# Optimization experiments

Measured on AMD Instinct MI355X. Metric: run time of the kernel, lower is better.

The kernel has to match this reference:

```python
import jax, jax.numpy as jnp
import numpy as np

V, D, B, L = 100000, 64, 4096, 200

def setup_inputs() -> dict:
    key = jax.random.key(0)
    ks = jax.random.split(key, 10)
    s = 0.05  # keep activations in a sane range for sigmoid
    return {
        "item_ids": jax.random.randint(ks[0], (B,), 0, V),
        "history": jax.random.randint(ks[1], (B, L), 0, V),
        "hist_len": jax.random.randint(ks[2], (B,), 1, L + 1),
        "emb_table": jax.random.normal(ks[3], (V, D), jnp.float32) * s,
        "aW1": jax.random.normal(ks[4], (3 * D, D), jnp.float32) * s,
        "ab1": jnp.zeros((D,), jnp.float32),
        "aW2": jax.random.normal(ks[5], (D, 1), jnp.float32) * s,
        "ab2": jnp.zeros((1,), jnp.float32),
        "fW1": jax.random.normal(ks[6], (3 * D, 128), jnp.float32) * s,
        "fb1": jnp.zeros((128,), jnp.float32),
        "fW2": jax.random.normal(ks[7], (128, 64), jnp.float32) * s,
        "fb2": jnp.zeros((64,), jnp.float32),
        "fW3": jax.random.normal(ks[8], (64, 1), jnp.float32) * s,
        "fb3": jnp.zeros((1,), jnp.float32),
    }

def reference(item_ids, history, hist_len, emb_table, aW1, ab1, aW2, ab2,
              fW1, fb1, fW2, fb2, fW3, fb3):
    target = emb_table[item_ids]                      # [B, D]
    hist = emb_table[history]                         # [B, L, D]
    # original pads short histories with zero rows -> zero the padded tail
    mask = (jnp.arange(hist.shape[1])[None, :] < hist_len[:, None]).astype(hist.dtype)
    hist = hist * mask[..., None]
    tgt = jnp.broadcast_to(target[:, None, :], hist.shape)     # [B, L, D]
    # attention_fc takes 3*D features: (hist, target, hist*target)
    feat = jnp.concatenate([hist, tgt, hist * tgt], axis=-1)   # [B, L, 3D]
    h = jax.nn.relu(feat @ aW1 + ab1)                 # [B, L, D]
    scores = (h @ aW2 + ab2)[..., 0]                  # [B, L]
    # faithful to original: softmax over full padded length (no length mask)
    w = jax.nn.softmax(scores, axis=1)
    pooled = jnp.einsum('bl,bld->bd', w, hist)        # [B, D]
    comb = jnp.concatenate([target, pooled, pooled - target], axis=-1)  # [B, 3D]
    z = jax.nn.relu(comb @ fW1 + fb1)
    z = jax.nn.relu(z @ fW2 + fb2)
    return jax.nn.sigmoid(z @ fW3 + fb3)              # [B, 1]
```

## Files before the change

### kernel.cpp

```cpp
#include <hip/hip_runtime.h>
#include <hip/hip_bf16.h>

#define NV 100000
#define ND 64
#define NB 4096
#define NL 200

typedef __bf16 bf16_t;
typedef __bf16 bf16x8 __attribute__((ext_vector_type(8)));
typedef float f32x4 __attribute__((ext_vector_type(4)));

#define HSTRIDE 72
#define MT 13

__global__ __launch_bounds__(256)
void din_kernel1(const int* __restrict__ item_ids,
                 const int* __restrict__ history,
                 const int* __restrict__ hist_len,
                 const float* __restrict__ emb,
                 const float* __restrict__ aW1,
                 const float* __restrict__ ab1,
                 const float* __restrict__ aW2,
                 float* __restrict__ comb_ws)
{
    __shared__ __align__(16) bf16_t histA[208 * HSTRIDE];
    __shared__ __align__(16) bf16_t wbT[64 * HSTRIDE];
    __shared__ float tgt[64];
    __shared__ float cb[64];
    __shared__ __align__(16) float scores[208];
    __shared__ float wts[208];
    __shared__ float pp[4 * 64];
    __shared__ float red[8];
    __shared__ float pooled[64];

    const int b   = blockIdx.x;
    const int tid = threadIdx.x;
    const int len = hist_len[b];

    if (tid < 64) tgt[tid] = emb[(long)item_ids[b] * ND + tid];

    {
        const int p     = tid & 3;
        const int lbase = tid >> 2;
        for (int pass = 0; pass < 4; ++pass) {
            int l = pass * 64 + lbase;
            if (l < 208) {
                bf16x8 o0 = (bf16x8)(bf16_t)0.f;
                bf16x8 o1 = (bf16x8)(bf16_t)0.f;
                if (l < NL && l < len) {
                    int idx = history[b * NL + l];
                    const float* src = emb + (long)idx * ND + p * 16;
                    f32x4 a0 = *(const f32x4*)(src);
                    f32x4 a1 = *(const f32x4*)(src + 4);
                    f32x4 a2 = *(const f32x4*)(src + 8);
                    f32x4 a3 = *(const f32x4*)(src + 12);
                    for (int i = 0; i < 4; ++i) {
                        o0[i]     = (bf16_t)a0[i];
                        o0[i + 4] = (bf16_t)a1[i];
                        o1[i]     = (bf16_t)a2[i];
                        o1[i + 4] = (bf16_t)a3[i];
                    }
                }
                bf16_t* dst = &histA[l * HSTRIDE + p * 16];
                *(bf16x8*)(dst)     = o0;
                *(bf16x8*)(dst + 8) = o1;
            }
        }
    }
    __syncthreads();

    {
        const int n  = tid & 63;
        const int kp = tid >> 6;
        float csum = 0.f;
        for (int i = 0; i < 16; ++i) {
            int k = kp * 16 + i;
            float tk = tgt[k];
            float w  = aW1[k * 64 + n] + tk * aW1[(128 + k) * 64 + n];
            wbT[n * HSTRIDE + k] = (bf16_t)w;
            csum += tk * aW1[(64 + k) * 64 + n];
        }
        pp[kp * 64 + n] = csum;
    }
    __syncthreads();
    if (tid < 64) cb[tid] = ab1[tid] + pp[tid] + pp[64 + tid] + pp[128 + tid] + pp[192 + tid];
    __syncthreads();

    {
        const int wave = tid >> 6;
        const int lane = tid & 63;
        const int col  = lane & 15;
        const int quad = lane >> 4;

        bf16x8 bfrag[4][2];
        for (int nt = 0; nt < 4; ++nt)
            for (int kb = 0; kb < 2; ++kb)
                bfrag[nt][kb] = *(const bf16x8*)&wbT[(nt * 16 + col) * HSTRIDE + kb * 32 + quad * 8];
        float cvals[4], a2vals[4];
        for (int nt = 0; nt < 4; ++nt) {
            cvals[nt]  = cb[nt * 16 + col];
            a2vals[nt] = aW2[nt * 16 + col];
        }

        for (int mt = wave; mt < MT; mt += 4) {
            const bf16_t* arow = &histA[(mt * 16 + col) * HSTRIDE + quad * 8];
            bf16x8 af0 = *(const bf16x8*)(arow);
            bf16x8 af1 = *(const bf16x8*)(arow + 32);
            float sc[4] = {0.f, 0.f, 0.f, 0.f};
            for (int nt = 0; nt < 4; ++nt) {
                f32x4 acc = {0.f, 0.f, 0.f, 0.f};
                acc = __builtin_amdgcn_mfma_f32_16x16x32_bf16(af0, bfrag[nt][0], acc, 0, 0, 0);
                acc = __builtin_amdgcn_mfma_f32_16x16x32_bf16(af1, bfrag[nt][1], acc, 0, 0, 0);
                for (int i = 0; i < 4; ++i) {
                    float h = acc[i] + cvals[nt];
                    h = h > 0.f ? h : 0.f;
                    sc[i] += h * a2vals[nt];
                }
            }
            for (int off = 1; off < 16; off <<= 1)
                for (int i = 0; i < 4; ++i)
                    sc[i] += __shfl_xor(sc[i], off, 64);
            if (col == 0) {
                f32x4 outv = {sc[0], sc[1], sc[2], sc[3]};
                *(f32x4*)&scores[mt * 16 + quad * 4] = outv;
            }
        }
    }
    __syncthreads();

    {
        float s = (tid < NL) ? scores[tid] : -1e30f;
        float m = s;
        for (int off = 32; off > 0; off >>= 1) m = fmaxf(m, __shfl_xor(m, off, 64));
        if ((tid & 63) == 0) red[tid >> 6] = m;
        __syncthreads();
        m = fmaxf(fmaxf(red[0], red[1]), fmaxf(red[2], red[3]));
        float e = (tid < NL) ? __expf(s - m) : 0.f;
        float ssum = e;
        for (int off = 32; off > 0; off >>= 1) ssum += __shfl_xor(ssum, off, 64);
        if ((tid & 63) == 0) red[4 + (tid >> 6)] = ssum;
        __syncthreads();
        float tot = red[4] + red[5] + red[6] + red[7];
        if (tid < NL) wts[tid] = e / tot;
    }
    __syncthreads();

    {
        const int wave = tid >> 6, lane = tid & 63;
        float acc = 0.f;
        for (int i = 0; i < 50; ++i) {
            int l = wave * 50 + i;
            float wl = wts[l];
            acc += wl * (float)histA[l * HSTRIDE + lane];
        }
        pp[wave * 64 + lane] = acc;
    }
    __syncthreads();
    if (tid < 64) pooled[tid] = pp[tid] + pp[64 + tid] + pp[128 + tid] + pp[192 + tid];
    __syncthreads();

    if (tid < 192) {
        float v;
        if (tid < 64)       v = tgt[tid];
        else if (tid < 128) v = pooled[tid - 64];
        else                v = pooled[tid - 128] - tgt[tid - 128];
        comb_ws[(long)b * 192 + tid] = v;
    }
}

__global__ __launch_bounds__(256)
void din_kernel2(const float* __restrict__ comb,
                 const float* __restrict__ fW1, const float* __restrict__ fb1,
                 const float* __restrict__ fW2, const float* __restrict__ fb2,
                 const float* __restrict__ fW3, const float* __restrict__ fb3,
                 float* __restrict__ out)
{
    __shared__ float z1s[16 * 130];
    __shared__ float z2s[16 * 66];
    const int tid = threadIdx.x;
    const int r   = tid >> 4;
    const int c   = tid & 15;
    const int row = blockIdx.x * 16 + r;

    float acc[8];
    for (int jj = 0; jj < 8; ++jj) acc[jj] = fb1[c * 8 + jj];
    for (int i = 0; i < 192; ++i) {
        float cm = comb[(long)row * 192 + i];
        const float* wr = fW1 + i * 128 + c * 8;
        f32x4 w0 = *(const f32x4*)(wr);
        f32x4 w1 = *(const f32x4*)(wr + 4);
        for (int jj = 0; jj < 4; ++jj) {
            acc[jj]     += cm * w0[jj];
            acc[jj + 4] += cm * w1[jj];
        }
    }
    for (int jj = 0; jj < 8; ++jj) z1s[r * 130 + c * 8 + jj] = fmaxf(acc[jj], 0.f);
    __syncthreads();

    float a2[4];
    for (int jj = 0; jj < 4; ++jj) a2[jj] = fb2[c * 4 + jj];
    for (int i = 0; i < 128; ++i) {
        float zv = z1s[r * 130 + i];
        f32x4 w = *(const f32x4*)(fW2 + i * 64 + c * 4);
        for (int jj = 0; jj < 4; ++jj) a2[jj] += zv * w[jj];
    }
    for (int jj = 0; jj < 4; ++jj) z2s[r * 66 + c * 4 + jj] = fmaxf(a2[jj], 0.f);
    __syncthreads();

    if (c == 0) {
        float s = fb3[0];
        for (int j = 0; j < 64; ++j) s += z2s[r * 66 + j] * fW3[j];
        out[row] = 1.f / (1.f + __expf(-s));
    }
}

extern "C" void kernel_launch(void* const* d_in, const int* in_sizes, int n_in,
                              void* d_out, int out_size, void* d_ws, size_t ws_size,
                              hipStream_t stream) {
    const int*   item_ids = (const int*)d_in[0];
    const int*   history  = (const int*)d_in[1];
    const int*   hist_len = (const int*)d_in[2];
    const float* emb      = (const float*)d_in[3];
    const float* aW1      = (const float*)d_in[4];
    const float* ab1      = (const float*)d_in[5];
    const float* aW2      = (const float*)d_in[6];
    const float* fW1      = (const float*)d_in[8];
    const float* fb1      = (const float*)d_in[9];
    const float* fW2      = (const float*)d_in[10];
    const float* fb2      = (const float*)d_in[11];
    const float* fW3      = (const float*)d_in[12];
    const float* fb3      = (const float*)d_in[13];

    float* comb = (float*)d_ws;

    din_kernel1<<<NB, 256, 0, stream>>>(item_ids, history, hist_len, emb,
                                        aW1, ab1, aW2, comb);
    din_kernel2<<<NB / 16, 256, 0, stream>>>(comb, fW1, fb1, fW2, fb2, fW3, fb3,
                                             (float*)d_out);
}
```

Baseline: 164.5 us.

## Stream history embeddings into MFMA registers instead of staging them in LDS

Drops the 208-row bf16 history tile from shared memory. Each wave now loads its embedding rows straight into registers in MFMA fragment layout and overlaps the first tile's gather with the weight-folding step. The pooling stage re-reads embeddings from global memory through saved indices, which adds a second gather but should cut LDS use and raise occupancy (launch bounds now ask for 5 blocks). It also vectorises the weight fold with shuffle reductions and rewrites the MLP kernel so each wave handles one row.

```diff
diff --git a/kernel.cpp b/kernel.cpp
--- a/kernel.cpp
+++ b/kernel.cpp
@@ -5,15 +5,14 @@
 #define ND 64
 #define NB 4096
 #define NL 200
+#define WST 72
 
 typedef __bf16 bf16_t;
 typedef __bf16 bf16x8 __attribute__((ext_vector_type(8)));
-typedef float f32x4 __attribute__((ext_vector_type(4)));
-
-#define HSTRIDE 72
-#define MT 13
-
-__global__ __launch_bounds__(256)
+typedef __bf16 bf16x4 __attribute__((ext_vector_type(4)));
+typedef float  f32x4  __attribute__((ext_vector_type(4)));
+
+__global__ __launch_bounds__(256, 5)
 void din_kernel1(const int* __restrict__ item_ids,
                  const int* __restrict__ history,
                  const int* __restrict__ hist_len,
@@ -23,122 +22,154 @@
                  const float* __restrict__ aW2,
                  float* __restrict__ comb_ws)
 {
-    __shared__ __align__(16) bf16_t histA[208 * HSTRIDE];
-    __shared__ __align__(16) bf16_t wbT[64 * HSTRIDE];
+    __shared__ __align__(16) bf16_t wbT[64 * WST];
+    __shared__ __align__(16) float scores[208];
+    __shared__ float wts[208];
+    __shared__ int   hidx[208];
+    __shared__ float pp[4 * 64];
     __shared__ float tgt[64];
     __shared__ float cb[64];
-    __shared__ __align__(16) float scores[208];
-    __shared__ float wts[208];
-    __shared__ float pp[4 * 64];
     __shared__ float red[8];
     __shared__ float pooled[64];
 
-    const int b   = blockIdx.x;
-    const int tid = threadIdx.x;
-    const int len = hist_len[b];
-
-    if (tid < 64) tgt[tid] = emb[(long)item_ids[b] * ND + tid];
+    const int b    = blockIdx.x;
+    const int tid  = threadIdx.x;
+    const int item = item_ids[b];
+    const int len  = hist_len[b];
+    const int wave = tid >> 6, lane = tid & 63;
+    const int col  = lane & 15, quad = lane >> 4;
+
+    if (tid < 64) tgt[tid] = emb[(long)item * ND + tid];
 
     {
-        const int p     = tid & 3;
-        const int lbase = tid >> 2;
-        for (int pass = 0; pass < 4; ++pass) {
-            int l = pass * 64 + lbase;
-            if (l < 208) {
-                bf16x8 o0 = (bf16x8)(bf16_t)0.f;
-                bf16x8 o1 = (bf16x8)(bf16_t)0.f;
-                if (l < NL && l < len) {
-                    int idx = history[b * NL + l];
-                    const float* src = emb + (long)idx * ND + p * 16;
-                    f32x4 a0 = *(const f32x4*)(src);
-                    f32x4 a1 = *(const f32x4*)(src + 4);
-                    f32x4 a2 = *(const f32x4*)(src + 8);
-                    f32x4 a3 = *(const f32x4*)(src + 12);
-                    for (int i = 0; i < 4; ++i) {
-                        o0[i]     = (bf16_t)a0[i];
-                        o0[i + 4] = (bf16_t)a1[i];
-                        o1[i]     = (bf16_t)a2[i];
-                        o1[i + 4] = (bf16_t)a3[i];
-                    }
-                }
-                bf16_t* dst = &histA[l * HSTRIDE + p * 16];
-                *(bf16x8*)(dst)     = o0;
-                *(bf16x8*)(dst + 8) = o1;
+        const int n4 = (tid & 15) * 4;
+        const int kp = tid >> 4;
+        f32x4 t4  = *(const f32x4*)(emb + (long)item * ND + kp * 4);
+        f32x4 wa0 = *(const f32x4*)(aW1 + (kp * 4 + 0) * 64 + n4);
+        f32x4 wa1 = *(const f32x4*)(aW1 + (kp * 4 + 1) * 64 + n4);
+        f32x4 wa2 = *(const f32x4*)(aW1 + (kp * 4 + 2) * 64 + n4);
+        f32x4 wa3 = *(const f32x4*)(aW1 + (kp * 4 + 3) * 64 + n4);
+        f32x4 wb0 = *(const f32x4*)(aW1 + (64 + kp * 4 + 0) * 64 + n4);
+        f32x4 wb1 = *(const f32x4*)(aW1 + (64 + kp * 4 + 1) * 64 + n4);
+        f32x4 wb2 = *(const f32x4*)(aW1 + (64 + kp * 4 + 2) * 64 + n4);
+        f32x4 wb3 = *(const f32x4*)(aW1 + (64 + kp * 4 + 3) * 64 + n4);
+        f32x4 wc0 = *(const f32x4*)(aW1 + (128 + kp * 4 + 0) * 64 + n4);
+        f32x4 wc1 = *(const f32x4*)(aW1 + (128 + kp * 4 + 1) * 64 + n4);
+        f32x4 wc2 = *(const f32x4*)(aW1 + (128 + kp * 4 + 2) * 64 + n4);
+        f32x4 wc3 = *(const f32x4*)(aW1 + (128 + kp * 4 + 3) * 64 + n4);
+
+        f32x4 c4;
+        #pragma unroll
+        for (int j = 0; j < 4; ++j) {
+            bf16x4 w;
+            w[0] = (bf16_t)(wa0[j] + t4[0] * wc0[j]);
+            w[1] = (bf16_t)(wa1[j] + t4[1] * wc1[j]);
+            w[2] = (bf16_t)(wa2[j] + t4[2] * wc2[j]);
+            w[3] = (bf16_t)(wa3[j] + t4[3] * wc3[j]);
+            *(bf16x4*)&wbT[(n4 + j) * WST + kp * 4] = w;
+            c4[j] = t4[0] * wb0[j] + t4[1] * wb1[j] + t4[2] * wb2[j] + t4[3] * wb3[j];
+        }
+        #pragma unroll
+        for (int j = 0; j < 4; ++j) {
+            c4[j] += __shfl_xor(c4[j], 16, 64);
+            c4[j] += __shfl_xor(c4[j], 32, 64);
+        }
+        if (lane < 16) *(f32x4*)&pp[wave * 64 + n4] = c4;
+    }
+
+    const int  l0   = wave * 16 + col;
+    const int  lc0  = l0 < NL ? l0 : NL - 1;
+    const int  idx0 = history[b * NL + lc0];
+    const bool v0   = l0 < len;
+    const float* s0 = emb + (long)idx0 * ND + quad * 8;
+    f32x4 pa0 = *(const f32x4*)(s0);
+    f32x4 pa1 = *(const f32x4*)(s0 + 4);
+    f32x4 pa2 = *(const f32x4*)(s0 + 32);
+    f32x4 pa3 = *(const f32x4*)(s0 + 36);
+
+    __syncthreads();
+
+    if (tid < 64) cb[tid] = ab1[tid] + pp[tid] + pp[64 + tid] + pp[128 + tid] + pp[192 + tid];
+
+    bf16x8 bfrag[4][2];
+    #pragma unroll
+    for (int nt = 0; nt < 4; ++nt)
+        #pragma unroll
+        for (int kb = 0; kb < 2; ++kb)
+            bfrag[nt][kb] = *(const bf16x8*)&wbT[(nt * 16 + col) * WST + kb * 32 + quad * 8];
+    float a2vals[4];
+    #pragma unroll
+    for (int nt = 0; nt < 4; ++nt) a2vals[nt] = aW2[nt * 16 + col];
+
+    __syncthreads();
+    float cvals[4];
+    #pragma unroll
+    for (int nt = 0; nt < 4; ++nt) cvals[nt] = cb[nt * 16 + col];
+
+    auto do_tile = [&](int mt, f32x4 a0, f32x4 a1, f32x4 a2, f32x4 a3, bool valid) {
+        bf16x8 af0, af1;
+        #pragma unroll
+        for (int i = 0; i < 4; ++i) {
+            af0[i]     = (bf16_t)a0[i];
+            af0[i + 4] = (bf16_t)a1[i];
+            af1[i]     = (bf16_t)a2[i];
+            af1[i + 4] = (bf16_t)a3[i];
+        }
+        if (!valid) { af0 = (bf16x8)(bf16_t)0.f; af1 = (bf16x8)(bf16_t)0.f; }
+        float sc[4] = {0.f, 0.f, 0.f, 0.f};
+        #pragma unroll
+        for (int nt = 0; nt < 4; ++nt) {
+            f32x4 acc = {0.f, 0.f, 0.f, 0.f};
+            acc = __builtin_amdgcn_mfma_f32_16x16x32_bf16(af0, bfrag[nt][0], acc, 0, 0, 0);
+            acc = __builtin_amdgcn_mfma_f32_16x16x32_bf16(af1, bfrag[nt][1], acc, 0, 0, 0);
+            #pragma unroll
+            for (int i = 0; i < 4; ++i) {
+                float h = acc[i] + cvals[nt];
+                h = h > 0.f ? h : 0.f;
+                sc[i] += h * a2vals[nt];
             }
         }
-    }
-    __syncthreads();
-
-    {
-        const int n  = tid & 63;
-        const int kp = tid >> 6;
-        float csum = 0.f;
-        for (int i = 0; i < 16; ++i) {
-            int k = kp * 16 + i;
-            float tk = tgt[k];
-            float w  = aW1[k * 64 + n] + tk * aW1[(128 + k) * 64 + n];
-            wbT[n * HSTRIDE + k] = (bf16_t)w;
-            csum += tk * aW1[(64 + k) * 64 + n];
-        }
-        pp[kp * 64 + n] = csum;
-    }
-    __syncthreads();
-    if (tid < 64) cb[tid] = ab1[tid] + pp[tid] + pp[64 + tid] + pp[128 + tid] + pp[192 + tid];
-    __syncthreads();
-
-    {
-        const int wave = tid >> 6;
-        const int lane = tid & 63;
-        const int col  = lane & 15;
-        const int quad = lane >> 4;
-
-        bf16x8 bfrag[4][2];
-        for (int nt = 0; nt < 4; ++nt)
-            for (int kb = 0; kb < 2; ++kb)
-                bfrag[nt][kb] = *(const bf16x8*)&wbT[(nt * 16 + col) * HSTRIDE + kb * 32 + quad * 8];
-        float cvals[4], a2vals[4];
-        for (int nt = 0; nt < 4; ++nt) {
-            cvals[nt]  = cb[nt * 16 + col];
-            a2vals[nt] = aW2[nt * 16 + col];
-        }
-
-        for (int mt = wave; mt < MT; mt += 4) {
-            const bf16_t* arow = &histA[(mt * 16 + col) * HSTRIDE + quad * 8];
-            bf16x8 af0 = *(const bf16x8*)(arow);
-            bf16x8 af1 = *(const bf16x8*)(arow + 32);
-            float sc[4] = {0.f, 0.f, 0.f, 0.f};
-            for (int nt = 0; nt < 4; ++nt) {
-                f32x4 acc = {0.f, 0.f, 0.f, 0.f};
-                acc = __builtin_amdgcn_mfma_f32_16x16x32_bf16(af0, bfrag[nt][0], acc, 0, 0, 0);
-                acc = __builtin_amdgcn_mfma_f32_16x16x32_bf16(af1, bfrag[nt][1], acc, 0, 0, 0);
-                for (int i = 0; i < 4; ++i) {
-                    float h = acc[i] + cvals[nt];
-                    h = h > 0.f ? h : 0.f;
-                    sc[i] += h * a2vals[nt];
-                }
-            }
-            for (int off = 1; off < 16; off <<= 1)
-                for (int i = 0; i < 4; ++i)
-                    sc[i] += __shfl_xor(sc[i], off, 64);
-            if (col == 0) {
-                f32x4 outv = {sc[0], sc[1], sc[2], sc[3]};
-                *(f32x4*)&scores[mt * 16 + quad * 4] = outv;
-            }
-        }
+        #pragma unroll
+        for (int off = 1; off < 16; off <<= 1)
+            #pragma unroll
+            for (int i = 0; i < 4; ++i) sc[i] += __shfl_xor(sc[i], off, 64);
+        if (col == 0) {
+            f32x4 outv = {sc[0], sc[1], sc[2], sc[3]};
+            *(f32x4*)&scores[mt * 16 + quad * 4] = outv;
+        }
+    };
+
+    if (quad == 0 && l0 < NL) hidx[l0] = idx0;
+    do_tile(wave, pa0, pa1, pa2, pa3, v0);
+
+    for (int mt = wave + 4; mt < 13; mt += 4) {
+        const int  l    = mt * 16 + col;
+        const int  lc   = l < NL ? l : NL - 1;
+        const int  idxv = history[b * NL + lc];
+        const bool vv   = l < len;
+        const float* sp = emb + (long)idxv * ND + quad * 8;
+        f32x4 a0 = *(const f32x4*)(sp);
+        f32x4 a1 = *(const f32x4*)(sp + 4);
+        f32x4 a2 = *(const f32x4*)(sp + 32);
+        f32x4 a3 = *(const f32x4*)(sp + 36);
+        if (quad == 0 && l < NL) hidx[l] = idxv;
+        do_tile(mt, a0, a1, a2, a3, vv);
     }
     __syncthreads();
 
     {
         float s = (tid < NL) ? scores[tid] : -1e30f;
         float m = s;
+        #pragma unroll
         for (int off = 32; off > 0; off >>= 1) m = fmaxf(m, __shfl_xor(m, off, 64));
-        if ((tid & 63) == 0) red[tid >> 6] = m;
+        if (lane == 0) red[wave] = m;
         __syncthreads();
         m = fmaxf(fmaxf(red[0], red[1]), fmaxf(red[2], red[3]));
         float e = (tid < NL) ? __expf(s - m) : 0.f;
         float ssum = e;
+        #pragma unroll
         for (int off = 32; off > 0; off >>= 1) ssum += __shfl_xor(ssum, off, 64);
-        if ((tid & 63) == 0) red[4 + (tid >> 6)] = ssum;
+        if (lane == 0) red[4 + wave] = ssum;
         __syncthreads();
         float tot = red[4] + red[5] + red[6] + red[7];
         if (tid < NL) wts[tid] = e / tot;
@@ -146,12 +177,10 @@
     __syncthreads();
 
     {
-        const int wave = tid >> 6, lane = tid & 63;
         float acc = 0.f;
-        for (int i = 0; i < 50; ++i) {
-            int l = wave * 50 + i;
-            float wl = wts[l];
-            acc += wl * (float)histA[l * HSTRIDE + lane];
+        for (int l = wave; l < NL; l += 4) {
+            float wl = (l < len) ? wts[l] : 0.f;
+            acc += wl * emb[(long)hidx[l] * ND + lane];
         }
         pp[wave * 64 + lane] = acc;
     }
@@ -175,43 +204,36 @@
                  const float* __restrict__ fW3, const float* __restrict__ fb3,
                  float* __restrict__ out)
 {
-    __shared__ float z1s[16 * 130];
-    __shared__ float z2s[16 * 66];
-    const int tid = threadIdx.x;
-    const int r   = tid >> 4;
-    const int c   = tid & 15;
-    const int row = blockIdx.x * 16 + r;
-
-    float acc[8];
-    for (int jj = 0; jj < 8; ++jj) acc[jj] = fb1[c * 8 + jj];
-    for (int i = 0; i < 192; ++i) {
-        float cm = comb[(long)row * 192 + i];
-        const float* wr = fW1 + i * 128 + c * 8;
-        f32x4 w0 = *(const f32x4*)(wr);
-        f32x4 w1 = *(const f32x4*)(wr + 4);
-        for (int jj = 0; jj < 4; ++jj) {
-            acc[jj]     += cm * w0[jj];
-            acc[jj + 4] += cm * w1[jj];
-        }
-    }
-    for (int jj = 0; jj < 8; ++jj) z1s[r * 130 + c * 8 + jj] = fmaxf(acc[jj], 0.f);
-    __syncthreads();
-
-    float a2[4];
-    for (int jj = 0; jj < 4; ++jj) a2[jj] = fb2[c * 4 + jj];
-    for (int i = 0; i < 128; ++i) {
-        float zv = z1s[r * 130 + i];
-        f32x4 w = *(const f32x4*)(fW2 + i * 64 + c * 4);
-        for (int jj = 0; jj < 4; ++jj) a2[jj] += zv * w[jj];
-    }
-    for (int jj = 0; jj < 4; ++jj) z2s[r * 66 + c * 4 + jj] = fmaxf(a2[jj], 0.f);
-    __syncthreads();
-
-    if (c == 0) {
-        float s = fb3[0];
-        for (int j = 0; j < 64; ++j) s += z2s[r * 66 + j] * fW3[j];
-        out[row] = 1.f / (1.f + __expf(-s));
-    }
+    __shared__ float z1s[4 * 128];
+    const int tid  = threadIdx.x;
+    const int wave = tid >> 6, lane = tid & 63;
+    const int row  = blockIdx.x * 4 + wave;
+
+    const float* crow = comb + (long)row * 192;
+    float acc0 = fb1[lane], acc1 = fb1[64 + lane];
+    #pragma unroll 4
+    for (int i4 = 0; i4 < 48; ++i4) {
+        f32x4 cm = *(const f32x4*)(crow + i4 * 4);
+        #pragma unroll
+        for (int u = 0; u < 4; ++u) {
+            const int i = i4 * 4 + u;
+            acc0 += cm[u] * fW1[i * 128 + lane];
+            acc1 += cm[u] * fW1[i * 128 + 64 + lane];
+        }
+    }
+    z1s[wave * 128 + lane]      = fmaxf(acc0, 0.f);
+    z1s[wave * 128 + 64 + lane] = fmaxf(acc1, 0.f);
+    __syncthreads();
+
+    float a2 = fb2[lane];
+    #pragma unroll 4
+    for (int i = 0; i < 128; ++i) a2 += z1s[wave * 128 + i] * fW2[i * 64 + lane];
+    float z2v = fmaxf(a2, 0.f);
+
+    float s = z2v * fW3[lane];
+    #pragma unroll
+    for (int off = 1; off < 64; off <<= 1) s += __shfl_xor(s, off, 64);
+    if (lane == 0) out[row] = 1.f / (1.f + __expf(-(s + fb3[0])));
 }
 
 extern "C" void kernel_launch(void* const* d_in, const int* in_sizes, int n_in,
@@ -235,6 +257,6 @@
 
     din_kernel1<<<NB, 256, 0, stream>>>(item_ids, history, hist_len, emb,
                                         aW1, ab1, aW2, comb);
-    din_kernel2<<<NB / 16, 256, 0, stream>>>(comb, fW1, fb1, fW2, fb2, fW3, fb3,
-                                             (float*)d_out);
+    din_kernel2<<<NB / 4, 256, 0, stream>>>(comb, fW1, fb1, fW2, fb2, fW3, fb3,
+                                            (float*)d_out);
 }
```

Result: slower. 215.7 us (+31.1%).
